# Optimization experiments

Measured on AMD Instinct MI355X. Metric: run time of the kernel, lower is better.

The kernel has to match this reference:

```python
import jax, jax.numpy as jnp
import numpy as np

NX = 768
N_HEAD = 12
N_CTX = 2048
BATCH = 4
EPS = 1e-5
NEG = -1000000000.0


def _layernorm(x, g, b):
    # NOTE: faithful to source bug: returns g + normalized + b (additive, not scale)
    u = jnp.mean(x, axis=-1, keepdims=True)
    s = jnp.mean((x - u) ** 2, axis=-1, keepdims=True)
    return g + (x - u) / jnp.sqrt(s + EPS) + b


def setup_inputs() -> dict:
    key = jax.random.key(0)
    ks = jax.random.split(key, 8)
    std = 0.02
    x = jax.random.normal(ks[0], (BATCH, N_CTX, NX), dtype=jnp.float32)
    w_attn = jax.random.normal(ks[1], (NX, 3 * NX), dtype=jnp.float32) * std
    b_attn = jnp.zeros((3 * NX,), jnp.float32)
    w_proj = jax.random.normal(ks[2], (NX, NX), dtype=jnp.float32) * std
    b_proj = jnp.zeros((NX,), jnp.float32)
    ln1_g = jnp.ones((NX,), jnp.float32)
    ln1_b = jnp.zeros((NX,), jnp.float32)
    w_fc = jax.random.normal(ks[3], (NX, 4 * NX), dtype=jnp.float32) * std
    b_fc = jnp.zeros((4 * NX,), jnp.float32)
    w_fc2 = jax.random.normal(ks[4], (4 * NX, NX), dtype=jnp.float32) * std
    b_fc2 = jnp.zeros((NX,), jnp.float32)
    ln2_g = jnp.ones((NX,), jnp.float32)
    ln2_b = jnp.zeros((NX,), jnp.float32)
    return dict(x=x, w_attn=w_attn, b_attn=b_attn, w_proj=w_proj, b_proj=b_proj,
                ln1_g=ln1_g, ln1_b=ln1_b, w_fc=w_fc, b_fc=b_fc,
                w_fc2=w_fc2, b_fc2=b_fc2, ln2_g=ln2_g, ln2_b=ln2_b)


def reference(x, w_attn, b_attn, w_proj, b_proj, ln1_g, ln1_b,
              w_fc, b_fc, w_fc2, b_fc2, ln2_g, ln2_b):
    B, S, D = x.shape
    dh = D // N_HEAD
    # --- attention (scale=False: no 1/sqrt(d)) ---
    qkv = x @ w_attn + b_attn                      # [B,S,3D]
    q, k, v = jnp.split(qkv, 3, axis=-1)
    q = q.reshape(B, S, N_HEAD, dh).transpose(0, 2, 1, 3)   # [B,H,S,dh]
    k = k.reshape(B, S, N_HEAD, dh).transpose(0, 2, 3, 1)   # [B,H,dh,S]
    v = v.reshape(B, S, N_HEAD, dh).transpose(0, 2, 1, 3)   # [B,H,S,dh]
    w = jnp.einsum('bhsd,bhdt->bhst', q, k)        # [B,H,S,S]
    mask = jnp.tril(jnp.ones((S, S), x.dtype))[None, None]
    w = w * mask + NEG * (1.0 - mask)
    w = jax.nn.softmax(w, axis=-1)
    a = jnp.einsum('bhst,bhtd->bhsd', w, v)        # [B,H,S,dh]
    a = a.transpose(0, 2, 1, 3).reshape(B, S, D)
    a = a @ w_proj + b_proj
    # dropout layers are identity (eval mode)
    n = _layernorm(x + a, ln1_g, ln1_b)
    # --- MLP (intended ReLU; source's nn.ReLU usage is a bug) ---
    h = jax.nn.relu(n @ w_fc + b_fc)
    m = h @ w_fc2 + b_fc2
    return _layernorm(n + m, ln2_g, ln2_b)
```

## Files before the change

kernel.cpp:

```cpp
#include <hip/hip_runtime.h>
#include <stdint.h>

#define NX 768
#define SEQ 2048
#define NHEAD 12
#define MROWS 8192
#define LN_EPS 1e-5f
#define MASK_NEG -1000000000.0f

typedef __bf16 bf16x8 __attribute__((ext_vector_type(8)));
typedef float f32x4 __attribute__((ext_vector_type(4)));

#define AS3(p)  ((__attribute__((address_space(3))) void*)(p))
#define AS1C(p) ((const __attribute__((address_space(1))) void*)(p))

__device__ __forceinline__ unsigned short f2bf(float f) {
  union { float f; unsigned int u; } v; v.f = f;
  unsigned int r = v.u + 0x7fffu + ((v.u >> 16) & 1u);
  return (unsigned short)(r >> 16);
}
__device__ __forceinline__ unsigned int f2bf_fast_u(float f) {
  union { float f; unsigned int u; } v; v.f = f;
  return (v.u + 0x8000u) >> 16;
}
__device__ __forceinline__ float bf2f(unsigned short u) {
  union { unsigned int u; float f; } v; v.u = ((unsigned int)u) << 16;
  return v.f;
}

__global__ void convert_f32_bf16(const float* __restrict__ in,
                                 unsigned short* __restrict__ out, int n4) {
  int i = blockIdx.x * blockDim.x + threadIdx.x;
  if (i >= n4) return;
  float4 v = ((const float4*)in)[i];
  ushort4 o;
  o.x = f2bf(v.x); o.y = f2bf(v.y); o.z = f2bf(v.z); o.w = f2bf(v.w);
  ((ushort4*)out)[i] = o;
}

__global__ void transpose_w(const float* __restrict__ w,
                            unsigned short* __restrict__ wt, int K, int N) {
  __shared__ float tile[32][33];
  int n0 = blockIdx.x * 32, k0 = blockIdx.y * 32;
  int tx = threadIdx.x, ty = threadIdx.y;
#pragma unroll
  for (int j = 0; j < 4; ++j)
    tile[ty + j * 8][tx] = w[(long)(k0 + ty + j * 8) * N + n0 + tx];
  __syncthreads();
#pragma unroll
  for (int j = 0; j < 4; ++j)
    wt[(long)(n0 + ty + j * 8) * K + k0 + tx] = f2bf(tile[tx][ty + j * 8]);
}

__global__ void transpose_v(const unsigned short* __restrict__ qkv,
                            unsigned short* __restrict__ vt) {
  __shared__ unsigned short tile[64][68];
  int s0 = blockIdx.x * 64;
  int bh = blockIdx.y, b = bh / NHEAD, h = bh % NHEAD;
  int tx = threadIdx.x, ty = threadIdx.y;
  const unsigned short* src = qkv + (long)b * SEQ * 2304 + 1536 + h * 64;
#pragma unroll
  for (int j = 0; j < 4; ++j) {
    int s = ty + j * 16;
    ushort4 vv = *(const ushort4*)(src + (long)(s0 + s) * 2304 + tx * 4);
    *(ushort4*)(&tile[s][tx * 4]) = vv;
  }
  __syncthreads();
  unsigned short* dst = vt + (long)bh * 64 * SEQ + s0;
#pragma unroll
  for (int j = 0; j < 4; ++j) {
    int d = ty + j * 16;
    ushort4 o;
    o.x = tile[tx * 4 + 0][d]; o.y = tile[tx * 4 + 1][d];
    o.z = tile[tx * 4 + 2][d]; o.w = tile[tx * 4 + 3][d];
    *(ushort4*)(dst + (long)d * SEQ + tx * 4) = o;
  }
}

template <int ACT, int BN>
__global__ __launch_bounds__(256) void gemm_bt(const unsigned short* __restrict__ A,
                                               const unsigned short* __restrict__ Bt,
                                               const float* __restrict__ bias,
                                               unsigned short* __restrict__ C,
                                               int Nsz, int K) {
  constexpr int ABUF = 128 * 64;
  constexpr int BBUF = BN * 64;
  constexpr int BUF = ABUF + BBUF;
  __shared__ __align__(16) unsigned short smem[2 * BUF];
  const int tid = threadIdx.x;
  const int w = tid >> 6, lane = tid & 63;
  const int l15 = lane & 15, quad = lane >> 4;
  constexpr int MT = (BN == 128) ? 4 : 2;
  const int wrow0 = (BN == 128) ? (w >> 1) * 64 : w * 32;
  const int wcol0 = (BN == 128) ? (w & 1) * 64 : 0;
  const long m0 = (long)blockIdx.x * 128;
  const long n0 = (long)blockIdx.y * BN;

  const int srow = tid >> 3;
  const int sg = tid & 7;

  const unsigned short* ap[4];
#pragma unroll
  for (int p = 0; p < 4; ++p) {
    int row = p * 32 + srow;
    ap[p] = A + (m0 + row) * (long)K + (sg ^ (row & 7)) * 8;
  }
  const unsigned short* bp[BN / 32];
#pragma unroll
  for (int p = 0; p < BN / 32; ++p) {
    int row = p * 32 + srow;
    bp[p] = Bt + (n0 + row) * (long)K + (sg ^ (row & 7)) * 8;
  }

  auto stage = [&](int kb) {
    unsigned short* As = smem + (kb & 1) * BUF;
    unsigned short* Bs = As + ABUF;
#pragma unroll
    for (int p = 0; p < 4; ++p) {
      __builtin_amdgcn_global_load_lds(AS1C(ap[p]), AS3(As + p * 2048 + w * 512), 16, 0, 0);
      ap[p] += 64;
    }
#pragma unroll
    for (int p = 0; p < BN / 32; ++p) {
      __builtin_amdgcn_global_load_lds(AS1C(bp[p]), AS3(Bs + p * 2048 + w * 512), 16, 0, 0);
      bp[p] += 64;
    }
  };

  f32x4 acc[MT][4] = {};
  const int nkb = K / 64;

  stage(0);
  for (int kb = 0; kb < nkb; ++kb) {
    __syncthreads();
    if (kb + 1 < nkb) stage(kb + 1);
    const unsigned short* As = smem + (kb & 1) * BUF;
    const unsigned short* Bs = As + ABUF;
#pragma unroll
    for (int s2 = 0; s2 < 2; ++s2) {
      const int phys = ((s2 * 4 + quad) ^ (l15 & 7)) * 8;
      bf16x8 af[MT], bfr[4];
#pragma unroll
      for (int mt = 0; mt < MT; ++mt)
        af[mt] = *(const bf16x8*)(As + (wrow0 + mt * 16 + l15) * 64 + phys);
#pragma unroll
      for (int nt = 0; nt < 4; ++nt)
        bfr[nt] = *(const bf16x8*)(Bs + (wcol0 + nt * 16 + l15) * 64 + phys);
#pragma unroll
      for (int mt = 0; mt < MT; ++mt)
#pragma unroll
        for (int nt = 0; nt < 4; ++nt)
          acc[mt][nt] = __builtin_amdgcn_mfma_f32_16x16x32_bf16(af[mt], bfr[nt], acc[mt][nt], 0, 0, 0);
    }
  }
  __syncthreads();

  unsigned short* Ew = smem + w * (16 * 72);
  const long gmB = m0 + wrow0;
  const long gnB = n0 + wcol0;
  float bv[4];
#pragma unroll
  for (int nt = 0; nt < 4; ++nt) bv[nt] = bias[gnB + nt * 16 + l15];
  const int prow = lane >> 3, pcol = (lane & 7) * 8;
#pragma unroll
  for (int mt = 0; mt < MT; ++mt) {
#pragma unroll
    for (int nt = 0; nt < 4; ++nt)
#pragma unroll
      for (int r = 0; r < 4; ++r) {
        float v = acc[mt][nt][r] + bv[nt];
        if (ACT == 1) v = fmaxf(v, 0.f);
        Ew[(quad * 4 + r) * 72 + nt * 16 + l15] = f2bf(v);
      }
#pragma unroll
    for (int ps = 0; ps < 2; ++ps) {
      int row = ps * 8 + prow;
      int4 t = *(const int4*)(Ew + row * 72 + pcol);
      *(int4*)(C + (gmB + mt * 16 + row) * (long)Nsz + gnB + pcol) = t;
    }
  }
}

__global__ __launch_bounds__(256) void attn_v7(const unsigned short* __restrict__ qkv,
                                               const unsigned short* __restrict__ vt,
                                               unsigned short* __restrict__ out) {
  const int blk = blockIdx.x;
  const int bh_lo = blk & 7;
  const int j = blk >> 3;
  const int bx = j & 15;
  const int bh = (j >> 4) * 8 + bh_lo;
  const int b = bh / NHEAD, h = bh % NHEAD;
  const int tid = threadIdx.x;
  const int w = tid >> 6, lane = tid & 63, l15 = lane & 15, quad = lane >> 4;

  __shared__ __align__(16) unsigned short Ks[2][64 * 64];
  __shared__ __align__(16) unsigned short Vs[2][64 * 64];
  __shared__ __align__(16) unsigned short Ps[4][16 * 64];

  const long rowbase = (long)b * SEQ;
  unsigned short* Pw = &Ps[w][0];
  const unsigned short* vbh = vt + (long)bh * 64 * SEQ;
  const float LOG2E = 1.4426950408889634f;

  const int krow = tid >> 3;
  const int kgo = (((tid & 7) ^ (krow & 7)) * 8);
  const unsigned short* kbase = qkv + rowbase * 2304L + 768 + h * 64;

  for (int pass = 0; pass < 2; ++pass) {
    const int qt = (pass == 0) ? bx : 31 - bx;
    const int niter = qt + 1;
    const int qrow = qt * 64 + w * 16 + l15;
    const int qg = qrow;

    bf16x8 qf[2];
#pragma unroll
    for (int s2 = 0; s2 < 2; ++s2) {
      int4 raw = *(const int4*)(qkv + (rowbase + qrow) * 2304L + h * 64 + s2 * 32 + quad * 8);
      const unsigned short* rp = (const unsigned short*)&raw;
#pragma unroll
      for (int j2 = 0; j2 < 8; ++j2)
        qf[s2][j2] = (__bf16)(bf2f(rp[j2]) * LOG2E);
    }

    const unsigned short* kp[2];
    const unsigned short* vp[2];
#pragma unroll
    for (int p = 0; p < 2; ++p) {
      kp[p] = kbase + (long)(p * 32 + krow) * 2304 + kgo;
      vp[p] = vbh + (long)(p * 32 + krow) * SEQ + kgo;
    }

    float l_sum = 0.f;
    f32x4 o_acc[4] = {};

    __syncthreads();
#pragma unroll
    for (int p = 0; p < 2; ++p) {
      __builtin_amdgcn_global_load_lds(AS1C(kp[p]), AS3(&Ks[0][0] + p * 2048 + w * 512), 16, 0, 0);
      __builtin_amdgcn_global_load_lds(AS1C(vp[p]), AS3(&Vs[0][0] + p * 2048 + w * 512), 16, 0, 0);
      kp[p] += 64 * 2304;
      vp[p] += 64;
    }

    for (int it = 0; it < niter; ++it) {
      __syncthreads();
      if (it + 1 < niter) {
        const int nb = (it + 1) & 1;
#pragma unroll
        for (int p = 0; p < 2; ++p) {
          __builtin_amdgcn_global_load_lds(AS1C(kp[p]), AS3(&Ks[nb][0] + p * 2048 + w * 512), 16, 0, 0);
          __builtin_amdgcn_global_load_lds(AS1C(vp[p]), AS3(&Vs[nb][0] + p * 2048 + w * 512), 16, 0, 0);
          kp[p] += 64 * 2304;
          vp[p] += 64;
        }
      }
      const unsigned short* Kc = &Ks[it & 1][0];
      const unsigned short* Vc = &Vs[it & 1][0];

      f32x4 st[4] = {};
#pragma unroll
      for (int nt = 0; nt < 4; ++nt) {
        int key = nt * 16 + l15;
#pragma unroll
        for (int s2 = 0; s2 < 2; ++s2) {
          int phys = (s2 * 4 + quad) ^ (key & 7);
          bf16x8 kf = *(const bf16x8*)(Kc + key * 64 + phys * 8);
          st[nt] = __builtin_amdgcn_mfma_f32_16x16x32_bf16(kf, qf[s2], st[nt], 0, 0, 0);
        }
      }

      if (it == niter - 1) {
#pragma unroll
        for (int nt = 0; nt < 4; ++nt) {
          int kg = it * 64 + nt * 16 + quad * 4;
#pragma unroll
          for (int r = 0; r < 4; ++r)
            if (kg + r > qg) st[nt][r] = MASK_NEG;
        }
      }

      float psum = 0.f;
#pragma unroll
      for (int nt = 0; nt < 4; ++nt)
#pragma unroll
        for (int r = 0; r < 4; ++r) {
          float p = __builtin_amdgcn_exp2f(st[nt][r]);
          st[nt][r] = p;
          psum += p;
        }
      psum += __shfl_xor(psum, 16);
      psum += __shfl_xor(psum, 32);
      l_sum += psum;

#pragma unroll
      for (int nt = 0; nt < 4; ++nt) {
        unsigned int lo = f2bf_fast_u(st[nt][0]) | (f2bf_fast_u(st[nt][1]) << 16);
        unsigned int hi = f2bf_fast_u(st[nt][2]) | (f2bf_fast_u(st[nt][3]) << 16);
        int g8 = (nt * 2 + (quad >> 1)) ^ (l15 & 7);
        uint2 pv; pv.x = lo; pv.y = hi;
        *(uint2*)(Pw + l15 * 64 + g8 * 8 + (quad & 1) * 4) = pv;
      }

#pragma unroll
      for (int c = 0; c < 2; ++c) {
        int phys = ((c * 4 + quad) ^ (l15 & 7)) * 8;
        bf16x8 pf = *(const bf16x8*)(Pw + l15 * 64 + phys);
#pragma unroll
        for (int ntd = 0; ntd < 4; ++ntd) {
          int d = ntd * 16 + l15;
          bf16x8 vf = *(const bf16x8*)(Vc + d * 64 + phys);
          o_acc[ntd] = __builtin_amdgcn_mfma_f32_16x16x32_bf16(pf, vf, o_acc[ntd], 0, 0, 0);
        }
      }
    }

#pragma unroll
    for (int r = 0; r < 4; ++r) {
      float lq = __shfl(l_sum, quad * 4 + r);
      float inv = 1.f / lq;
      int q = qt * 64 + w * 16 + quad * 4 + r;
#pragma unroll
      for (int ntd = 0; ntd < 4; ++ntd) {
        int d = ntd * 16 + l15;
        out[(rowbase + q) * (long)NX + h * 64 + d] = f2bf(o_acc[ntd][r] * inv);
      }
    }
  }
}

__global__ __launch_bounds__(256) void add_ln(const float* __restrict__ x_f,
                                              const unsigned short* __restrict__ x_b,
                                              const unsigned short* __restrict__ y_b,
                                              const float* __restrict__ g,
                                              const float* __restrict__ beta,
                                              float* __restrict__ out_f,
                                              unsigned short* __restrict__ out_b) {
  const int row = blockIdx.x, t = threadIdx.x;
  const long base = (long)row * NX;
  float v[3];
#pragma unroll
  for (int j = 0; j < 3; ++j) {
    int i = t + j * 256;
    float a = x_f ? x_f[base + i] : bf2f(x_b[base + i]);
    v[j] = a + bf2f(y_b[base + i]);
  }
  __shared__ float red[4];
  int wv = t >> 6, ln = t & 63;

  float ssum = v[0] + v[1] + v[2];
#pragma unroll
  for (int sh = 32; sh >= 1; sh >>= 1) ssum += __shfl_xor(ssum, sh);
  if (ln == 0) red[wv] = ssum;
  __syncthreads();
  float u = (red[0] + red[1] + red[2] + red[3]) * (1.f / NX);
  __syncthreads();

  float d0 = v[0] - u, d1 = v[1] - u, d2 = v[2] - u;
  float sq = d0 * d0 + d1 * d1 + d2 * d2;
#pragma unroll
  for (int sh = 32; sh >= 1; sh >>= 1) sq += __shfl_xor(sq, sh);
  if (ln == 0) red[wv] = sq;
  __syncthreads();
  float s = (red[0] + red[1] + red[2] + red[3]) * (1.f / NX);
  float rinv = rsqrtf(s + LN_EPS);

  float dd[3] = {d0, d1, d2};
#pragma unroll
  for (int j = 0; j < 3; ++j) {
    int i = t + j * 256;
    float o = g[i] + dd[j] * rinv + beta[i];
    if (out_f) out_f[base + i] = o;
    else out_b[base + i] = f2bf(o);
  }
}

extern "C" void kernel_launch(void* const* d_in, const int* in_sizes, int n_in,
                              void* d_out, int out_size, void* d_ws, size_t ws_size,
                              hipStream_t stream) {
  const float* x      = (const float*)d_in[0];
  const float* w_attn = (const float*)d_in[1];
  const float* b_attn = (const float*)d_in[2];
  const float* w_proj = (const float*)d_in[3];
  const float* b_proj = (const float*)d_in[4];
  const float* ln1_g  = (const float*)d_in[5];
  const float* ln1_b  = (const float*)d_in[6];
  const float* w_fc   = (const float*)d_in[7];
  const float* b_fc   = (const float*)d_in[8];
  const float* w_fc2  = (const float*)d_in[9];
  const float* b_fc2  = (const float*)d_in[10];
  const float* ln2_g  = (const float*)d_in[11];
  const float* ln2_b  = (const float*)d_in[12];
  float* out = (float*)d_out;

  char* ws = (char*)d_ws;
  size_t off = 0;
  auto alloc = [&](size_t bytes) {
    char* p = ws + off;
    off += (bytes + 255) & ~(size_t)255;
    return p;
  };
  unsigned short* xb      = (unsigned short*)alloc((size_t)MROWS * NX * 2);
  unsigned short* wt_attn = (unsigned short*)alloc((size_t)2304 * 768 * 2);
  unsigned short* wt_proj = (unsigned short*)alloc((size_t)768 * 768 * 2);
  unsigned short* wt_fc   = (unsigned short*)alloc((size_t)3072 * 768 * 2);
  unsigned short* wt_fc2  = (unsigned short*)alloc((size_t)768 * 3072 * 2);
  unsigned short* qkv     = (unsigned short*)alloc((size_t)MROWS * 3072 * 2);
  unsigned short* hbuf    = qkv;
  unsigned short* abuf    = (unsigned short*)alloc((size_t)MROWS * NX * 2);
  unsigned short* mbuf    = abuf;
  unsigned short* nbuf    = (unsigned short*)alloc((size_t)MROWS * NX * 2);
  unsigned short* vtb     = nbuf;
  unsigned short* pout    = xb;

  convert_f32_bf16<<<(MROWS * NX / 4 + 255) / 256, 256, 0, stream>>>(x, xb, MROWS * NX / 4);
  transpose_w<<<dim3(2304 / 32, 768 / 32), dim3(32, 8), 0, stream>>>(w_attn, wt_attn, 768, 2304);
  transpose_w<<<dim3(768 / 32, 768 / 32), dim3(32, 8), 0, stream>>>(w_proj, wt_proj, 768, 768);
  transpose_w<<<dim3(3072 / 32, 768 / 32), dim3(32, 8), 0, stream>>>(w_fc, wt_fc, 768, 3072);
  transpose_w<<<dim3(768 / 32, 3072 / 32), dim3(32, 8), 0, stream>>>(w_fc2, wt_fc2, 3072, 768);

  gemm_bt<0, 64><<<dim3(MROWS / 128, 2304 / 64), 256, 0, stream>>>(xb, wt_attn, b_attn, qkv, 2304, 768);
  transpose_v<<<dim3(SEQ / 64, 48), dim3(16, 16), 0, stream>>>(qkv, vtb);
  attn_v7<<<768, 256, 0, stream>>>(qkv, vtb, abuf);
  gemm_bt<0, 64><<<dim3(MROWS / 128, 768 / 64), 256, 0, stream>>>(abuf, wt_proj, b_proj, pout, 768, 768);
  add_ln<<<MROWS, 256, 0, stream>>>(x, nullptr, pout, ln1_g, ln1_b, nullptr, nbuf);
  gemm_bt<1, 128><<<dim3(MROWS / 128, 3072 / 128), 256, 0, stream>>>(nbuf, wt_fc, b_fc, hbuf, 3072, 768);
  gemm_bt<0, 64><<<dim3(MROWS / 128, 768 / 64), 256, 0, stream>>>(hbuf, wt_fc2, b_fc2, mbuf, 768, 3072);
  add_ln<<<MROWS, 256, 0, stream>>>(nullptr, nbuf, mbuf, ln2_g, ln2_b, out, nullptr);
}
```

Baseline: 341.4 us.

## Fuse prep kernels, shrink GEMM K-tile, and use 2-wave attention with 32 rows/wave

Merges the input conversion and the four weight transposes into one prep_all launch to cut launch overhead. Reworks gemm_bt to a single 128x64 tile with a K-step of 32 and no XOR swizzle, which also drops the 128-wide FC1 variant. Rewrites attention so each block has 2 waves, each handling 32 query rows, so every K/V fragment read feeds two MFMAs. The risks are LDS bank conflicts from the unswizzled GEMM layout, twice as many barriers per K loop, and lower occupancy for attention.

```diff
diff --git a/kernel.cpp b/kernel.cpp
--- a/kernel.cpp
+++ b/kernel.cpp
@@ -28,21 +28,12 @@
   return v.f;
 }
 
-__global__ void convert_f32_bf16(const float* __restrict__ in,
-                                 unsigned short* __restrict__ out, int n4) {
-  int i = blockIdx.x * blockDim.x + threadIdx.x;
-  if (i >= n4) return;
-  float4 v = ((const float4*)in)[i];
-  ushort4 o;
-  o.x = f2bf(v.x); o.y = f2bf(v.y); o.z = f2bf(v.z); o.w = f2bf(v.w);
-  ((ushort4*)out)[i] = o;
-}
-
-__global__ void transpose_w(const float* __restrict__ w,
-                            unsigned short* __restrict__ wt, int K, int N) {
+__device__ __forceinline__ void tw_tile(const float* __restrict__ w,
+                                        unsigned short* __restrict__ wt,
+                                        int K, int N, int bx, int by, int tid) {
   __shared__ float tile[32][33];
-  int n0 = blockIdx.x * 32, k0 = blockIdx.y * 32;
-  int tx = threadIdx.x, ty = threadIdx.y;
+  int n0 = bx * 32, k0 = by * 32;
+  int tx = tid & 31, ty = tid >> 5;
 #pragma unroll
   for (int j = 0; j < 4; ++j)
     tile[ty + j * 8][tx] = w[(long)(k0 + ty + j * 8) * N + n0 + tx];
@@ -50,6 +41,38 @@
 #pragma unroll
   for (int j = 0; j < 4; ++j)
     wt[(long)(n0 + ty + j * 8) * K + k0 + tx] = f2bf(tile[tx][ty + j * 8]);
+}
+
+__global__ __launch_bounds__(256) void prep_all(const float* __restrict__ x,
+                                                unsigned short* __restrict__ xb,
+                                                const float* __restrict__ w_attn,
+                                                unsigned short* __restrict__ wt_attn,
+                                                const float* __restrict__ w_proj,
+                                                unsigned short* __restrict__ wt_proj,
+                                                const float* __restrict__ w_fc,
+                                                unsigned short* __restrict__ wt_fc,
+                                                const float* __restrict__ w_fc2,
+                                                unsigned short* __restrict__ wt_fc2) {
+  const int blk = blockIdx.x, tid = threadIdx.x;
+  if (blk < 6144) {
+    int i = blk * 256 + tid;
+    float4 v = ((const float4*)x)[i];
+    ushort4 o;
+    o.x = f2bf(v.x); o.y = f2bf(v.y); o.z = f2bf(v.z); o.w = f2bf(v.w);
+    ((ushort4*)xb)[i] = o;
+  } else if (blk < 6144 + 1728) {
+    int r = blk - 6144;
+    tw_tile(w_attn, wt_attn, 768, 2304, r % 72, r / 72, tid);
+  } else if (blk < 6144 + 1728 + 576) {
+    int r = blk - (6144 + 1728);
+    tw_tile(w_proj, wt_proj, 768, 768, r % 24, r / 24, tid);
+  } else if (blk < 6144 + 1728 + 576 + 2304) {
+    int r = blk - (6144 + 1728 + 576);
+    tw_tile(w_fc, wt_fc, 768, 3072, r % 96, r / 96, tid);
+  } else {
+    int r = blk - (6144 + 1728 + 576 + 2304);
+    tw_tile(w_fc2, wt_fc2, 3072, 768, r % 24, r / 24, tid);
+  }
 }
 
 __global__ void transpose_v(const unsigned short* __restrict__ qkv,
@@ -77,58 +100,45 @@
   }
 }
 
-template <int ACT, int BN>
+template <int ACT>
 __global__ __launch_bounds__(256) void gemm_bt(const unsigned short* __restrict__ A,
                                                const unsigned short* __restrict__ Bt,
                                                const float* __restrict__ bias,
                                                unsigned short* __restrict__ C,
                                                int Nsz, int K) {
-  constexpr int ABUF = 128 * 64;
-  constexpr int BBUF = BN * 64;
+  constexpr int ABUF = 128 * 32;
+  constexpr int BBUF = 64 * 32;
   constexpr int BUF = ABUF + BBUF;
   __shared__ __align__(16) unsigned short smem[2 * BUF];
   const int tid = threadIdx.x;
   const int w = tid >> 6, lane = tid & 63;
   const int l15 = lane & 15, quad = lane >> 4;
-  constexpr int MT = (BN == 128) ? 4 : 2;
-  const int wrow0 = (BN == 128) ? (w >> 1) * 64 : w * 32;
-  const int wcol0 = (BN == 128) ? (w & 1) * 64 : 0;
   const long m0 = (long)blockIdx.x * 128;
-  const long n0 = (long)blockIdx.y * BN;
-
-  const int srow = tid >> 3;
-  const int sg = tid & 7;
-
-  const unsigned short* ap[4];
-#pragma unroll
-  for (int p = 0; p < 4; ++p) {
-    int row = p * 32 + srow;
-    ap[p] = A + (m0 + row) * (long)K + (sg ^ (row & 7)) * 8;
-  }
-  const unsigned short* bp[BN / 32];
-#pragma unroll
-  for (int p = 0; p < BN / 32; ++p) {
-    int row = p * 32 + srow;
-    bp[p] = Bt + (n0 + row) * (long)K + (sg ^ (row & 7)) * 8;
-  }
+  const long n0 = (long)blockIdx.y * 64;
+
+  const int srow = lane >> 2;
+  const int sgo = (lane & 3) * 8;
+
+  const unsigned short* ap[2];
+#pragma unroll
+  for (int i = 0; i < 2; ++i)
+    ap[i] = A + (m0 + w * 32 + i * 16 + srow) * (long)K + sgo;
+  const unsigned short* bp = Bt + (n0 + w * 16 + srow) * (long)K + sgo;
 
   auto stage = [&](int kb) {
     unsigned short* As = smem + (kb & 1) * BUF;
     unsigned short* Bs = As + ABUF;
 #pragma unroll
-    for (int p = 0; p < 4; ++p) {
-      __builtin_amdgcn_global_load_lds(AS1C(ap[p]), AS3(As + p * 2048 + w * 512), 16, 0, 0);
-      ap[p] += 64;
-    }
-#pragma unroll
-    for (int p = 0; p < BN / 32; ++p) {
-      __builtin_amdgcn_global_load_lds(AS1C(bp[p]), AS3(Bs + p * 2048 + w * 512), 16, 0, 0);
-      bp[p] += 64;
-    }
+    for (int i = 0; i < 2; ++i) {
+      __builtin_amdgcn_global_load_lds(AS1C(ap[i]), AS3(As + w * 1024 + i * 512), 16, 0, 0);
+      ap[i] += 32;
+    }
+    __builtin_amdgcn_global_load_lds(AS1C(bp), AS3(Bs + w * 512), 16, 0, 0);
+    bp += 32;
   };
 
-  f32x4 acc[MT][4] = {};
-  const int nkb = K / 64;
+  f32x4 acc[2][4] = {};
+  const int nkb = K / 32;
 
   stage(0);
   for (int kb = 0; kb < nkb; ++kb) {
@@ -136,34 +146,29 @@
     if (kb + 1 < nkb) stage(kb + 1);
     const unsigned short* As = smem + (kb & 1) * BUF;
     const unsigned short* Bs = As + ABUF;
-#pragma unroll
-    for (int s2 = 0; s2 < 2; ++s2) {
-      const int phys = ((s2 * 4 + quad) ^ (l15 & 7)) * 8;
-      bf16x8 af[MT], bfr[4];
-#pragma unroll
-      for (int mt = 0; mt < MT; ++mt)
-        af[mt] = *(const bf16x8*)(As + (wrow0 + mt * 16 + l15) * 64 + phys);
+    bf16x8 af[2], bfr[4];
+#pragma unroll
+    for (int mt = 0; mt < 2; ++mt)
+      af[mt] = *(const bf16x8*)(As + (w * 32 + mt * 16 + l15) * 32 + quad * 8);
+#pragma unroll
+    for (int nt = 0; nt < 4; ++nt)
+      bfr[nt] = *(const bf16x8*)(Bs + (nt * 16 + l15) * 32 + quad * 8);
+#pragma unroll
+    for (int mt = 0; mt < 2; ++mt)
 #pragma unroll
       for (int nt = 0; nt < 4; ++nt)
-        bfr[nt] = *(const bf16x8*)(Bs + (wcol0 + nt * 16 + l15) * 64 + phys);
-#pragma unroll
-      for (int mt = 0; mt < MT; ++mt)
-#pragma unroll
-        for (int nt = 0; nt < 4; ++nt)
-          acc[mt][nt] = __builtin_amdgcn_mfma_f32_16x16x32_bf16(af[mt], bfr[nt], acc[mt][nt], 0, 0, 0);
-    }
+        acc[mt][nt] = __builtin_amdgcn_mfma_f32_16x16x32_bf16(af[mt], bfr[nt], acc[mt][nt], 0, 0, 0);
   }
   __syncthreads();
 
   unsigned short* Ew = smem + w * (16 * 72);
-  const long gmB = m0 + wrow0;
-  const long gnB = n0 + wcol0;
+  const long gmB = m0 + w * 32;
   float bv[4];
 #pragma unroll
-  for (int nt = 0; nt < 4; ++nt) bv[nt] = bias[gnB + nt * 16 + l15];
+  for (int nt = 0; nt < 4; ++nt) bv[nt] = bias[n0 + nt * 16 + l15];
   const int prow = lane >> 3, pcol = (lane & 7) * 8;
 #pragma unroll
-  for (int mt = 0; mt < MT; ++mt) {
+  for (int mt = 0; mt < 2; ++mt) {
 #pragma unroll
     for (int nt = 0; nt < 4; ++nt)
 #pragma unroll
@@ -176,68 +181,71 @@
     for (int ps = 0; ps < 2; ++ps) {
       int row = ps * 8 + prow;
       int4 t = *(const int4*)(Ew + row * 72 + pcol);
-      *(int4*)(C + (gmB + mt * 16 + row) * (long)Nsz + gnB + pcol) = t;
-    }
-  }
-}
-
-__global__ __launch_bounds__(256) void attn_v7(const unsigned short* __restrict__ qkv,
+      *(int4*)(C + (gmB + mt * 16 + row) * (long)Nsz + n0 + pcol) = t;
+    }
+  }
+}
+
+__global__ __launch_bounds__(128) void attn_v8(const unsigned short* __restrict__ qkv,
                                                const unsigned short* __restrict__ vt,
                                                unsigned short* __restrict__ out) {
   const int blk = blockIdx.x;
   const int bh_lo = blk & 7;
-  const int j = blk >> 3;
-  const int bx = j & 15;
-  const int bh = (j >> 4) * 8 + bh_lo;
+  const int jj = blk >> 3;
+  const int bx = jj & 15;
+  const int bh = (jj >> 4) * 8 + bh_lo;
   const int b = bh / NHEAD, h = bh % NHEAD;
   const int tid = threadIdx.x;
   const int w = tid >> 6, lane = tid & 63, l15 = lane & 15, quad = lane >> 4;
 
   __shared__ __align__(16) unsigned short Ks[2][64 * 64];
   __shared__ __align__(16) unsigned short Vs[2][64 * 64];
-  __shared__ __align__(16) unsigned short Ps[4][16 * 64];
+  __shared__ __align__(16) unsigned short Ps[2][32 * 64];
 
   const long rowbase = (long)b * SEQ;
   unsigned short* Pw = &Ps[w][0];
   const unsigned short* vbh = vt + (long)bh * 64 * SEQ;
   const float LOG2E = 1.4426950408889634f;
 
-  const int krow = tid >> 3;
-  const int kgo = (((tid & 7) ^ (krow & 7)) * 8);
+  const int srow8 = lane >> 3;
+  const int kgo = (((lane & 7) ^ srow8) * 8);
   const unsigned short* kbase = qkv + rowbase * 2304L + 768 + h * 64;
 
   for (int pass = 0; pass < 2; ++pass) {
     const int qt = (pass == 0) ? bx : 31 - bx;
     const int niter = qt + 1;
-    const int qrow = qt * 64 + w * 16 + l15;
-    const int qg = qrow;
-
-    bf16x8 qf[2];
-#pragma unroll
-    for (int s2 = 0; s2 < 2; ++s2) {
-      int4 raw = *(const int4*)(qkv + (rowbase + qrow) * 2304L + h * 64 + s2 * 32 + quad * 8);
-      const unsigned short* rp = (const unsigned short*)&raw;
-#pragma unroll
-      for (int j2 = 0; j2 < 8; ++j2)
-        qf[s2][j2] = (__bf16)(bf2f(rp[j2]) * LOG2E);
-    }
-
-    const unsigned short* kp[2];
-    const unsigned short* vp[2];
-#pragma unroll
-    for (int p = 0; p < 2; ++p) {
-      kp[p] = kbase + (long)(p * 32 + krow) * 2304 + kgo;
-      vp[p] = vbh + (long)(p * 32 + krow) * SEQ + kgo;
-    }
-
-    float l_sum = 0.f;
-    f32x4 o_acc[4] = {};
+
+    bf16x8 qf[2][2];
+#pragma unroll
+    for (int g = 0; g < 2; ++g) {
+      const int qrow = qt * 64 + w * 32 + g * 16 + l15;
+#pragma unroll
+      for (int s2 = 0; s2 < 2; ++s2) {
+        int4 raw = *(const int4*)(qkv + (rowbase + qrow) * 2304L + h * 64 + s2 * 32 + quad * 8);
+        const unsigned short* rp = (const unsigned short*)&raw;
+#pragma unroll
+        for (int j2 = 0; j2 < 8; ++j2)
+          qf[g][s2][j2] = (__bf16)(bf2f(rp[j2]) * LOG2E);
+      }
+    }
+
+    const unsigned short* kp[4];
+    const unsigned short* vp[4];
+#pragma unroll
+    for (int p = 0; p < 4; ++p) {
+      int row = p * 16 + w * 8 + srow8;
+      kp[p] = kbase + (long)row * 2304 + kgo;
+      vp[p] = vbh + (long)row * SEQ + kgo;
+    }
+
+    float l_sum[2] = {0.f, 0.f};
+    f32x4 o_acc[2][4] = {};
 
     __syncthreads();
 #pragma unroll
-    for (int p = 0; p < 2; ++p) {
-      __builtin_amdgcn_global_load_lds(AS1C(kp[p]), AS3(&Ks[0][0] + p * 2048 + w * 512), 16, 0, 0);
-      __builtin_amdgcn_global_load_lds(AS1C(vp[p]), AS3(&Vs[0][0] + p * 2048 + w * 512), 16, 0, 0);
+    for (int p = 0; p < 4; ++p) {
+      __builtin_amdgcn_global_load_lds(AS1C(kp[p]), AS3(&Ks[0][0] + p * 1024 + w * 512), 16, 0, 0);
+      __builtin_amdgcn_global_load_lds(AS1C(vp[p]), AS3(&Vs[0][0] + p * 1024 + w * 512), 16, 0, 0);
       kp[p] += 64 * 2304;
       vp[p] += 64;
     }
@@ -247,9 +255,9 @@
       if (it + 1 < niter) {
         const int nb = (it + 1) & 1;
 #pragma unroll
-        for (int p = 0; p < 2; ++p) {
-          __builtin_amdgcn_global_load_lds(AS1C(kp[p]), AS3(&Ks[nb][0] + p * 2048 + w * 512), 16, 0, 0);
-          __builtin_amdgcn_global_load_lds(AS1C(vp[p]), AS3(&Vs[nb][0] + p * 2048 + w * 512), 16, 0, 0);
+        for (int p = 0; p < 4; ++p) {
+          __builtin_amdgcn_global_load_lds(AS1C(kp[p]), AS3(&Ks[nb][0] + p * 1024 + w * 512), 16, 0, 0);
+          __builtin_amdgcn_global_load_lds(AS1C(vp[p]), AS3(&Vs[nb][0] + p * 1024 + w * 512), 16, 0, 0);
           kp[p] += 64 * 2304;
           vp[p] += 64;
         }
@@ -257,7 +265,7 @@
       const unsigned short* Kc = &Ks[it & 1][0];
       const unsigned short* Vc = &Vs[it & 1][0];
 
-      f32x4 st[4] = {};
+      f32x4 st[2][4] = {};
 #pragma unroll
       for (int nt = 0; nt < 4; ++nt) {
         int key = nt * 16 + l15;
@@ -265,66 +273,83 @@
         for (int s2 = 0; s2 < 2; ++s2) {
           int phys = (s2 * 4 + quad) ^ (key & 7);
           bf16x8 kf = *(const bf16x8*)(Kc + key * 64 + phys * 8);
-          st[nt] = __builtin_amdgcn_mfma_f32_16x16x32_bf16(kf, qf[s2], st[nt], 0, 0, 0);
+#pragma unroll
+          for (int g = 0; g < 2; ++g)
+            st[g][nt] = __builtin_amdgcn_mfma_f32_16x16x32_bf16(kf, qf[g][s2], st[g][nt], 0, 0, 0);
         }
       }
 
       if (it == niter - 1) {
 #pragma unroll
+        for (int g = 0; g < 2; ++g) {
+          const int qg = qt * 64 + w * 32 + g * 16 + l15;
+#pragma unroll
+          for (int nt = 0; nt < 4; ++nt) {
+            int kg = it * 64 + nt * 16 + quad * 4;
+#pragma unroll
+            for (int r = 0; r < 4; ++r)
+              if (kg + r > qg) st[g][nt][r] = MASK_NEG;
+          }
+        }
+      }
+
+#pragma unroll
+      for (int g = 0; g < 2; ++g) {
+        float psum = 0.f;
+#pragma unroll
+        for (int nt = 0; nt < 4; ++nt)
+#pragma unroll
+          for (int r = 0; r < 4; ++r) {
+            float p = __builtin_amdgcn_exp2f(st[g][nt][r]);
+            st[g][nt][r] = p;
+            psum += p;
+          }
+        psum += __shfl_xor(psum, 16);
+        psum += __shfl_xor(psum, 32);
+        l_sum[g] += psum;
+      }
+
+#pragma unroll
+      for (int g = 0; g < 2; ++g)
+#pragma unroll
         for (int nt = 0; nt < 4; ++nt) {
-          int kg = it * 64 + nt * 16 + quad * 4;
-#pragma unroll
-          for (int r = 0; r < 4; ++r)
-            if (kg + r > qg) st[nt][r] = MASK_NEG;
-        }
-      }
-
-      float psum = 0.f;
-#pragma unroll
-      for (int nt = 0; nt < 4; ++nt)
-#pragma unroll
-        for (int r = 0; r < 4; ++r) {
-          float p = __builtin_amdgcn_exp2f(st[nt][r]);
-          st[nt][r] = p;
-          psum += p;
-        }
-      psum += __shfl_xor(psum, 16);
-      psum += __shfl_xor(psum, 32);
-      l_sum += psum;
-
-#pragma unroll
-      for (int nt = 0; nt < 4; ++nt) {
-        unsigned int lo = f2bf_fast_u(st[nt][0]) | (f2bf_fast_u(st[nt][1]) << 16);
-        unsigned int hi = f2bf_fast_u(st[nt][2]) | (f2bf_fast_u(st[nt][3]) << 16);
-        int g8 = (nt * 2 + (quad >> 1)) ^ (l15 & 7);
-        uint2 pv; pv.x = lo; pv.y = hi;
-        *(uint2*)(Pw + l15 * 64 + g8 * 8 + (quad & 1) * 4) = pv;
-      }
+          unsigned int lo = f2bf_fast_u(st[g][nt][0]) | (f2bf_fast_u(st[g][nt][1]) << 16);
+          unsigned int hi = f2bf_fast_u(st[g][nt][2]) | (f2bf_fast_u(st[g][nt][3]) << 16);
+          int g8 = (nt * 2 + (quad >> 1)) ^ (l15 & 7);
+          uint2 pv; pv.x = lo; pv.y = hi;
+          *(uint2*)(Pw + (g * 16 + l15) * 64 + g8 * 8 + (quad & 1) * 4) = pv;
+        }
 
 #pragma unroll
       for (int c = 0; c < 2; ++c) {
-        int phys = ((c * 4 + quad) ^ (l15 & 7)) * 8;
-        bf16x8 pf = *(const bf16x8*)(Pw + l15 * 64 + phys);
+        bf16x8 pf[2];
+#pragma unroll
+        for (int g = 0; g < 2; ++g)
+          pf[g] = *(const bf16x8*)(Pw + (g * 16 + l15) * 64 + (((c * 4 + quad) ^ (l15 & 7)) * 8));
 #pragma unroll
         for (int ntd = 0; ntd < 4; ++ntd) {
           int d = ntd * 16 + l15;
-          bf16x8 vf = *(const bf16x8*)(Vc + d * 64 + phys);
-          o_acc[ntd] = __builtin_amdgcn_mfma_f32_16x16x32_bf16(pf, vf, o_acc[ntd], 0, 0, 0);
-        }
-      }
-    }
-
-#pragma unroll
-    for (int r = 0; r < 4; ++r) {
-      float lq = __shfl(l_sum, quad * 4 + r);
-      float inv = 1.f / lq;
-      int q = qt * 64 + w * 16 + quad * 4 + r;
-#pragma unroll
-      for (int ntd = 0; ntd < 4; ++ntd) {
-        int d = ntd * 16 + l15;
-        out[(rowbase + q) * (long)NX + h * 64 + d] = f2bf(o_acc[ntd][r] * inv);
-      }
-    }
+          bf16x8 vf = *(const bf16x8*)(Vc + d * 64 + (((c * 4 + quad) ^ (d & 7)) * 8));
+#pragma unroll
+          for (int g = 0; g < 2; ++g)
+            o_acc[g][ntd] = __builtin_amdgcn_mfma_f32_16x16x32_bf16(pf[g], vf, o_acc[g][ntd], 0, 0, 0);
+        }
+      }
+    }
+
+#pragma unroll
+    for (int g = 0; g < 2; ++g)
+#pragma unroll
+      for (int r = 0; r < 4; ++r) {
+        float lq = __shfl(l_sum[g], quad * 4 + r);
+        float inv = 1.f / lq;
+        int q = qt * 64 + w * 32 + g * 16 + quad * 4 + r;
+#pragma unroll
+        for (int ntd = 0; ntd < 4; ++ntd) {
+          int d = ntd * 16 + l15;
+          out[(rowbase + q) * (long)NX + h * 64 + d] = f2bf(o_acc[g][ntd][r] * inv);
+        }
+      }
   }
 }
 
@@ -412,18 +437,15 @@
   unsigned short* vtb     = nbuf;
   unsigned short* pout    = xb;
 
-  convert_f32_bf16<<<(MROWS * NX / 4 + 255) / 256, 256, 0, stream>>>(x, xb, MROWS * NX / 4);
-  transpose_w<<<dim3(2304 / 32, 768 / 32), dim3(32, 8), 0, stream>>>(w_attn, wt_attn, 768, 2304);
-  transpose_w<<<dim3(768 / 32, 768 / 32), dim3(32, 8), 0, stream>>>(w_proj, wt_proj, 768, 768);
-  transpose_w<<<dim3(3072 / 32, 768 / 32), dim3(32, 8), 0, stream>>>(w_fc, wt_fc, 768, 3072);
-  transpose_w<<<dim3(768 / 32, 3072 / 32), dim3(32, 8), 0, stream>>>(w_fc2, wt_fc2, 3072, 768);
-
-  gemm_bt<0, 64><<<dim3(MROWS / 128, 2304 / 64), 256, 0, stream>>>(xb, wt_attn, b_attn, qkv, 2304, 768);
+  prep_all<<<13056, 256, 0, stream>>>(x, xb, w_attn, wt_attn, w_proj, wt_proj,
+                                      w_fc, wt_fc, w_fc2, wt_fc2);
+
+  gemm_bt<0><<<dim3(MROWS / 128, 2304 / 64), 256, 0, stream>>>(xb, wt_attn, b_attn, qkv, 2304, 768);
   transpose_v<<<dim3(SEQ / 64, 48), dim3(16, 16), 0, stream>>>(qkv, vtb);
-  attn_v7<<<768, 256, 0, stream>>>(qkv, vtb, abuf);
-  gemm_bt<0, 64><<<dim3(MROWS / 128, 768 / 64), 256, 0, stream>>>(abuf, wt_proj, b_proj, pout, 768, 768);
+  attn_v8<<<768, 128, 0, stream>>>(qkv, vtb, abuf);
+  gemm_bt<0><<<dim3(MROWS / 128, 768 / 64), 256, 0, stream>>>(abuf, wt_proj, b_proj, pout, 768, 768);
   add_ln<<<MROWS, 256, 0, stream>>>(x, nullptr, pout, ln1_g, ln1_b, nullptr, nbuf);
-  gemm_bt<1, 128><<<dim3(MROWS / 128, 3072 / 128), 256, 0, stream>>>(nbuf, wt_fc, b_fc, hbuf, 3072, 768);
-  gemm_bt<0, 64><<<dim3(MROWS / 128, 768 / 64), 256, 0, stream>>>(hbuf, wt_fc2, b_fc2, mbuf, 768, 3072);
+  gemm_bt<1><<<dim3(MROWS / 128, 3072 / 64), 256, 0, stream>>>(nbuf, wt_fc, b_fc, hbuf, 3072, 768);
+  gemm_bt<0><<<dim3(MROWS / 128, 768 / 64), 256, 0, stream>>>(hbuf, wt_fc2, b_fc2, mbuf, 768, 3072);
   add_ln<<<MROWS, 256, 0, stream>>>(nullptr, nbuf, mbuf, ln2_g, ln2_b, out, nullptr);
 }
```

After: 387.6 us. 1.14x slower.
